# Kernel optimization log

Measured on AMD Instinct MI355X. Metric: run time of the kernel, lower is better.

Reference implementation:

```python
import jax, jax.numpy as jnp
import numpy as np

N_NODES = 50000
N_EDGES = 800000
D = 128


def _gcn_layer(x, src, dst, deg_inv_sqrt, W, b, n_nodes):
    # GCNConv: X' = D^{-1/2} (A + I) D^{-1/2} X W + b   (PyG default, self-loops added)
    h = x @ W  # [N, D]
    norm = deg_inv_sqrt[src] * deg_inv_sqrt[dst]  # [E+N]
    msgs = h[src] * norm[:, None]  # [E+N, D] gather + scale
    out = jax.ops.segment_sum(msgs, dst, num_segments=n_nodes)  # scatter-add
    return out + b


def setup_inputs() -> dict:
    key = jax.random.key(0)
    k1, k2, k3, k4 = jax.random.split(key, 4)
    x = jax.random.normal(k1, (N_NODES, D), dtype=jnp.float32)
    edge_index = jax.random.randint(k2, (2, N_EDGES), 0, N_NODES, dtype=jnp.int64)
    scale = 1.0 / np.sqrt(D)
    W1 = jax.random.normal(k3, (D, D), dtype=jnp.float32) * scale
    b1 = jnp.zeros((D,), dtype=jnp.float32)
    W2 = jax.random.normal(k4, (D, D), dtype=jnp.float32) * scale
    b2 = jnp.zeros((D,), dtype=jnp.float32)
    return {"x": x, "edge_index": edge_index, "W1": W1, "b1": b1, "W2": W2, "b2": b2}


def reference(x, edge_index, W1, b1, W2, b2):
    n_nodes = x.shape[0]
    # add self-loops once (same graph both layers)
    loop = jnp.arange(n_nodes, dtype=edge_index.dtype)
    src = jnp.concatenate([edge_index[0], loop])
    dst = jnp.concatenate([edge_index[1], loop])
    deg = jax.ops.segment_sum(jnp.ones_like(dst, dtype=x.dtype), dst, num_segments=n_nodes)
    deg_inv_sqrt = jnp.where(deg > 0, jax.lax.rsqrt(deg), 0.0)

    h = _gcn_layer(x, src, dst, deg_inv_sqrt, W1, b1, n_nodes)
    h = jax.nn.relu(h)
    h = _gcn_layer(h, src, dst, deg_inv_sqrt, W2, b2, n_nodes)
    h = jax.nn.relu(h)
    return h
```

## Files before the change

### kernel.cpp

```cpp
#include <hip/hip_runtime.h>

#define N_NODES 50000
#define N_EDGES 800000
#define D 128
#define NB 392
#define CHUNK 2048
#define NBKT 391
#define LHM (NBKT * NB)
#define NSB ((LHM + 255) / 256)
#define GB ((N_NODES + 127) / 128)

typedef unsigned int uint32;
typedef unsigned short ushort;
typedef __attribute__((ext_vector_type(8))) short s8v;
typedef __attribute__((ext_vector_type(4))) float f4v;

__device__ __forceinline__ ushort f2bf(float f) {
    unsigned u = __float_as_uint(f);
    u += 0x7FFFu + ((u >> 16) & 1u);
    return (ushort)(u >> 16);
}
__device__ __forceinline__ float bf_lo(uint32 u) { return __uint_as_float(u << 16); }
__device__ __forceinline__ float bf_hi(uint32 u) { return __uint_as_float(u & 0xFFFF0000u); }

__device__ __forceinline__ int block_incl_scan(int v, int t) {
    int lane = t & 63, wv = t >> 6;
    int incl = v;
    #pragma unroll
    for (int off = 1; off < 64; off <<= 1) {
        int u = __shfl_up(incl, off, 64);
        if (lane >= off) incl += u;
    }
    __shared__ int wsums[4];
    if (lane == 63) wsums[wv] = incl;
    __syncthreads();
    int add = 0;
    if (wv > 0) add += wsums[0];
    if (wv > 1) add += wsums[1];
    if (wv > 2) add += wsums[2];
    return incl + add;
}

__global__ __launch_bounds__(256) void phaseA_kernel(const int* __restrict__ dst,
                                                     int* __restrict__ histM,
                                                     const float* __restrict__ W1,
                                                     const float* __restrict__ W2,
                                                     ushort* __restrict__ W1t,
                                                     ushort* __restrict__ W2t) {
    int t = threadIdx.x, blk = blockIdx.x;
    if (blk >= NB) {
        const float* W = (blk - NB) ? W2 : W1;
        ushort* Wt = (blk - NB) ? W2t : W1t;
        #pragma unroll
        for (int it = 0; it < 16; it++) {
            int fid = t + it * 256;
            int k = fid >> 5;
            int n0 = (fid & 31) * 4;
            float4 w = ((const float4*)W)[fid];
            Wt[(n0 + 0) * D + k] = f2bf(w.x);
            Wt[(n0 + 1) * D + k] = f2bf(w.y);
            Wt[(n0 + 2) * D + k] = f2bf(w.z);
            Wt[(n0 + 3) * D + k] = f2bf(w.w);
        }
        return;
    }
    __shared__ int lc[NBKT];
    for (int i = t; i < NBKT; i += 256) lc[i] = 0;
    __syncthreads();
    int e0 = blk * CHUNK;
    #pragma unroll
    for (int j = 0; j < 8; j++) {
        int e = e0 + t + j * 256;
        if (e < N_EDGES) atomicAdd(&lc[dst[e] >> 7], 1);
    }
    __syncthreads();
    for (int i = t; i < NBKT; i += 256)
        histM[i * NB + blk] = lc[i];
}

__global__ __launch_bounds__(256) void scan1g(const int* __restrict__ in,
                                              int* __restrict__ out,
                                              int* __restrict__ bsum) {
    int t = threadIdx.x, blk = blockIdx.x;
    int i = blk * 256 + t;
    int v = (i < LHM) ? in[i] : 0;
    int incl = block_incl_scan(v, t);
    if (i < LHM) out[i] = incl - v;
    if (t == 255) bsum[blk] = incl;
}

__global__ __launch_bounds__(256) void scan23g(int* __restrict__ out,
                                               const int* __restrict__ bsum) {
    int t = threadIdx.x, blk = blockIdx.x;
    int local = 0;
    for (int i = t; i < blk; i += 256) local += bsum[i];
    int lane = t & 63, wv = t >> 6;
    #pragma unroll
    for (int off = 32; off > 0; off >>= 1) local += __shfl_down(local, off, 64);
    __shared__ int ws[4];
    if (lane == 0) ws[wv] = local;
    __syncthreads();
    int boff = ws[0] + ws[1] + ws[2] + ws[3];
    int i = blk * 256 + t;
    if (i < LHM) out[i] += boff;
}

__global__ __launch_bounds__(256) void phaseC_kernel(const int* __restrict__ src,
                                                     const int* __restrict__ dst,
                                                     const int* __restrict__ base,
                                                     uint32* __restrict__ edgeTmp) {
    __shared__ int cur[NBKT];
    int t = threadIdx.x, blk = blockIdx.x;
    for (int i = t; i < NBKT; i += 256) cur[i] = base[i * NB + blk];
    __syncthreads();
    int e0 = blk * CHUNK;
    #pragma unroll
    for (int j = 0; j < 8; j++) {
        int e = e0 + t + j * 256;
        if (e < N_EDGES) {
            uint32 s = (uint32)src[e], d = (uint32)dst[e];
            int p = atomicAdd(&cur[d >> 7], 1);
            edgeTmp[p] = (s << 16) | d;
        }
    }
}

__global__ __launch_bounds__(256) void phaseD_kernel(const uint32* __restrict__ edgeTmp,
                                                     const int* __restrict__ base,
                                                     int* __restrict__ rowstart,
                                                     float* __restrict__ dis,
                                                     ushort* __restrict__ e16) {
    __shared__ int cnt[128];
    __shared__ int cur[128];
    int t = threadIdx.x, b = blockIdx.x;
    int beg = base[b * NB];
    int end = (b == NBKT - 1) ? N_EDGES : base[(b + 1) * NB];
    if (t < 128) cnt[t] = 0;
    __syncthreads();
    for (int p = beg + t; p < end; p += 256)
        atomicAdd(&cnt[edgeTmp[p] & 127], 1);
    __syncthreads();
    int c = (t < 128) ? cnt[t] : 0;
    int incl = block_incl_scan(c, t);
    int excl = incl - c;
    int node = b * 128 + t;
    if (t < 128) {
        if (node <= N_NODES) rowstart[node] = beg + excl;
        if (node < N_NODES) dis[node] = rsqrtf((float)(c + 1));
        cur[t] = excl;
    }
    __syncthreads();
    for (int p = beg + t; p < end; p += 256) {
        uint32 u = edgeTmp[p];
        int r = atomicAdd(&cur[u & 127], 1);
        e16[beg + r] = (ushort)(u >> 16);
    }
}

template<bool BF16IN>
__global__ __launch_bounds__(256) void gemm_mfma(const void* __restrict__ Xv,
                                                 const ushort* __restrict__ Wt,
                                                 const float* __restrict__ dis,
                                                 ushort* __restrict__ Hb) {
    __shared__ ushort Cs[128 * 136];
    int t = threadIdx.x;
    int wv = t >> 6, lane = t & 63;
    int q = lane >> 4, m = lane & 15;
    int rbase = blockIdx.x * 128 + wv * 32;
    f4v zero = {0.f, 0.f, 0.f, 0.f};
    f4v acc[2][8];
    #pragma unroll
    for (int mt = 0; mt < 2; mt++)
        #pragma unroll
        for (int n = 0; n < 8; n++) acc[mt][n] = zero;

    #pragma unroll
    for (int kt = 0; kt < 4; kt++) {
        int k0 = kt * 32 + q * 8;
        s8v a[2];
        #pragma unroll
        for (int mt = 0; mt < 2; mt++) {
            int row = rbase + mt * 16 + m;
            if (row >= N_NODES) row = N_NODES - 1;
            if (BF16IN) {
                const ushort* xp = (const ushort*)Xv + (size_t)row * D + k0;
                a[mt] = *(const s8v*)xp;
            } else {
                const float* xp = (const float*)Xv + (size_t)row * D + k0;
                float4 u0 = *(const float4*)xp;
                float4 u1 = *(const float4*)(xp + 4);
                s8v av;
                av[0] = (short)f2bf(u0.x); av[1] = (short)f2bf(u0.y);
                av[2] = (short)f2bf(u0.z); av[3] = (short)f2bf(u0.w);
                av[4] = (short)f2bf(u1.x); av[5] = (short)f2bf(u1.y);
                av[6] = (short)f2bf(u1.z); av[7] = (short)f2bf(u1.w);
                a[mt] = av;
            }
        }
        #pragma unroll
        for (int n = 0; n < 8; n++) {
            s8v b = *(const s8v*)(Wt + (size_t)(n * 16 + m) * D + k0);
            acc[0][n] = __builtin_amdgcn_mfma_f32_16x16x32_bf16(a[0], b, acc[0][n], 0, 0, 0);
            acc[1][n] = __builtin_amdgcn_mfma_f32_16x16x32_bf16(a[1], b, acc[1][n], 0, 0, 0);
        }
    }
    float disv[2][4];
    #pragma unroll
    for (int mt = 0; mt < 2; mt++)
        #pragma unroll
        for (int r = 0; r < 4; r++) {
            int row = rbase + mt * 16 + q * 4 + r;
            if (row >= N_NODES) row = N_NODES - 1;
            disv[mt][r] = dis[row];
        }
    #pragma unroll
    for (int mt = 0; mt < 2; mt++)
        #pragma unroll
        for (int n = 0; n < 8; n++)
            #pragma unroll
            for (int r = 0; r < 4; r++) {
                int row = wv * 32 + mt * 16 + q * 4 + r;
                Cs[row * 136 + n * 16 + m] = f2bf(acc[mt][n][r] * disv[mt][r]);
            }
    __syncthreads();
    int gbase = blockIdx.x * 128;
    #pragma unroll
    for (int it = 0; it < 8; it++) {
        int cid = t + it * 256;
        int row = cid >> 4, off = (cid & 15) * 8;
        int grow = gbase + row;
        if (grow < N_NODES) {
            s8v v = *(const s8v*)(Cs + row * 136 + off);
            *(s8v*)(Hb + (size_t)grow * D + off) = v;
        }
    }
}

__device__ __forceinline__ void acc8(float* a, uint4 v) {
    a[0] += bf_lo(v.x); a[1] += bf_hi(v.x);
    a[2] += bf_lo(v.y); a[3] += bf_hi(v.y);
    a[4] += bf_lo(v.z); a[5] += bf_hi(v.z);
    a[6] += bf_lo(v.w); a[7] += bf_hi(v.w);
}

template<bool BF16OUT>
__global__ __launch_bounds__(256) void aggr_kernel(const uint4* __restrict__ Hb4,
                                                   const float* __restrict__ dis,
                                                   const int* __restrict__ rowstart,
                                                   const ushort* __restrict__ e16,
                                                   const float* __restrict__ bias,
                                                   void* __restrict__ Hout) {
    int t = threadIdx.x;
    int li = t & 15;
    int n = blockIdx.x * 16 + (t >> 4);
    float dn = dis[n];
    float a[8];
    {
        uint4 sv = Hb4[(size_t)n * 16 + li];
        a[0] = bf_lo(sv.x); a[1] = bf_hi(sv.x);
        a[2] = bf_lo(sv.y); a[3] = bf_hi(sv.y);
        a[4] = bf_lo(sv.z); a[5] = bf_hi(sv.z);
        a[6] = bf_lo(sv.w); a[7] = bf_hi(sv.w);
    }
    int beg = rowstart[n], end = rowstart[n + 1];
    int p = beg;
    for (; p + 7 < end; p += 8) {
        int s[8];
        #pragma unroll
        for (int j = 0; j < 8; j++) s[j] = e16[p + j];
        uint4 v[8];
        #pragma unroll
        for (int j = 0; j < 8; j++) v[j] = Hb4[(size_t)s[j] * 16 + li];
        #pragma unroll
        for (int j = 0; j < 8; j++) acc8(a, v[j]);
    }
    for (; p + 3 < end; p += 4) {
        int s0 = e16[p + 0], s1 = e16[p + 1], s2 = e16[p + 2], s3 = e16[p + 3];
        uint4 v0 = Hb4[(size_t)s0 * 16 + li];
        uint4 v1 = Hb4[(size_t)s1 * 16 + li];
        uint4 v2 = Hb4[(size_t)s2 * 16 + li];
        uint4 v3 = Hb4[(size_t)s3 * 16 + li];
        acc8(a, v0); acc8(a, v1); acc8(a, v2); acc8(a, v3);
    }
    for (; p < end; p++) {
        uint4 v0 = Hb4[(size_t)e16[p] * 16 + li];
        acc8(a, v0);
    }
    const float4* b4 = (const float4*)bias;
    float4 bb0 = b4[li * 2], bb1 = b4[li * 2 + 1];
    float r0 = fmaxf(fmaf(dn, a[0], bb0.x), 0.f);
    float r1 = fmaxf(fmaf(dn, a[1], bb0.y), 0.f);
    float r2 = fmaxf(fmaf(dn, a[2], bb0.z), 0.f);
    float r3 = fmaxf(fmaf(dn, a[3], bb0.w), 0.f);
    float r4 = fmaxf(fmaf(dn, a[4], bb1.x), 0.f);
    float r5 = fmaxf(fmaf(dn, a[5], bb1.y), 0.f);
    float r6 = fmaxf(fmaf(dn, a[6], bb1.z), 0.f);
    float r7 = fmaxf(fmaf(dn, a[7], bb1.w), 0.f);
    if (BF16OUT) {
        uint4 o;
        o.x = (uint32)f2bf(r0) | ((uint32)f2bf(r1) << 16);
        o.y = (uint32)f2bf(r2) | ((uint32)f2bf(r3) << 16);
        o.z = (uint32)f2bf(r4) | ((uint32)f2bf(r5) << 16);
        o.w = (uint32)f2bf(r6) | ((uint32)f2bf(r7) << 16);
        ((uint4*)Hout)[(size_t)n * 16 + li] = o;
    } else {
        float4* H4 = (float4*)Hout;
        float4 o0; o0.x = r0; o0.y = r1; o0.z = r2; o0.w = r3;
        float4 o1; o1.x = r4; o1.y = r5; o1.z = r6; o1.w = r7;
        H4[(size_t)n * 32 + li * 2]     = o0;
        H4[(size_t)n * 32 + li * 2 + 1] = o1;
    }
}

extern "C" void kernel_launch(void* const* d_in, const int* in_sizes, int n_in,
                              void* d_out, int out_size, void* d_ws, size_t ws_size,
                              hipStream_t stream) {
    const float* x  = (const float*)d_in[0];
    const int*   ei = (const int*)d_in[1];
    const float* W1 = (const float*)d_in[2];
    const float* b1 = (const float*)d_in[3];
    const float* W2 = (const float*)d_in[4];
    const float* b2 = (const float*)d_in[5];
    float* out = (float*)d_out;

    char* ws = (char*)d_ws;
    size_t off = 0;
    auto alloc = [&](size_t bytes) -> void* {
        void* p = ws + off;
        off += (bytes + 255) & ~(size_t)255;
        return p;
    };
    int*    histM    = (int*)alloc((size_t)LHM * 4);
    int*    base     = (int*)alloc((size_t)LHM * 4);
    int*    bsum     = (int*)alloc((size_t)NSB * 4);
    int*    rowstart = (int*)alloc((size_t)(N_NODES + 1) * 4);
    float*  dis      = (float*)alloc((size_t)N_NODES * 4);
    uint32* edgeTmp  = (uint32*)alloc((size_t)N_EDGES * 4);
    ushort* e16      = (ushort*)alloc((size_t)N_EDGES * 2);
    ushort* Hb       = (ushort*)alloc((size_t)N_NODES * D * 2);
    ushort* HO1      = (ushort*)alloc((size_t)N_NODES * D * 2);
    ushort* W1t      = (ushort*)alloc((size_t)D * D * 2);
    ushort* W2t      = (ushort*)alloc((size_t)D * D * 2);

    const int* src = ei;
    const int* dst = ei + N_EDGES;

    phaseA_kernel<<<NB + 2, 256, 0, stream>>>(dst, histM, W1, W2, W1t, W2t);
    scan1g<<<NSB, 256, 0, stream>>>(histM, base, bsum);
    scan23g<<<NSB, 256, 0, stream>>>(base, bsum);
    phaseC_kernel<<<NB, 256, 0, stream>>>(src, dst, base, edgeTmp);
    phaseD_kernel<<<NBKT, 256, 0, stream>>>(edgeTmp, base, rowstart, dis, e16);

    gemm_mfma<false><<<GB, 256, 0, stream>>>(x, W1t, dis, Hb);
    aggr_kernel<true><<<N_NODES / 16, 256, 0, stream>>>((const uint4*)Hb, dis, rowstart,
                                                        e16, b1, HO1);
    gemm_mfma<true><<<GB, 256, 0, stream>>>(HO1, W2t, dis, Hb);
    aggr_kernel<false><<<N_NODES / 16, 256, 0, stream>>>((const uint4*)Hb, dis, rowstart,
                                                         e16, b2, out);
}
```

Before: 204.8 us.

## Sort nodes by degree and remap aggregation to balance wavefront work

Adds three kernels that histogram node in-degrees, scan the bins, and build a permutation that groups nodes of similar degree into the same wavefront. The aggregation kernel is restructured so each node is handled by 4 lanes looping over four feature quarters, with 16 nodes per wave and blocks built from the degree-sorted permutation. The goal is to cut lane divergence from unequal neighbour counts within a wave. The cost is extra preprocessing launches and a serial quarter loop that re-reads edge indices four times per node.

```diff
diff --git a/kernel.cpp b/kernel.cpp
--- a/kernel.cpp
+++ b/kernel.cpp
@@ -9,6 +9,9 @@
 #define LHM (NBKT * NB)
 #define NSB ((LHM + 255) / 256)
 #define GB ((N_NODES + 127) / 128)
+#define AGB 782
+#define NBIN 128
+#define BPAD 32
 
 typedef unsigned int uint32;
 typedef unsigned short ushort;
@@ -46,8 +49,13 @@
                                                      const float* __restrict__ W1,
                                                      const float* __restrict__ W2,
                                                      ushort* __restrict__ W1t,
-                                                     ushort* __restrict__ W2t) {
+                                                     ushort* __restrict__ W2t,
+                                                     int* __restrict__ dhist) {
     int t = threadIdx.x, blk = blockIdx.x;
+    if (blk == NB + 2) {
+        for (int i = t; i < NBIN * BPAD; i += 256) dhist[i] = 0;
+        return;
+    }
     if (blk >= NB) {
         const float* W = (blk - NB) ? W2 : W1;
         ushort* Wt = (blk - NB) ? W2t : W1t;
@@ -154,6 +162,63 @@
         uint32 u = edgeTmp[p];
         int r = atomicAdd(&cur[u & 127], 1);
         e16[beg + r] = (ushort)(u >> 16);
+    }
+}
+
+__global__ __launch_bounds__(256) void histdeg_kernel(const int* __restrict__ rowstart,
+                                                      int* __restrict__ dhist) {
+    __shared__ int dh[NBIN];
+    int t = threadIdx.x;
+    if (t < NBIN) dh[t] = 0;
+    __syncthreads();
+    int n = blockIdx.x * 256 + t;
+    if (n < N_NODES) {
+        int deg = rowstart[n + 1] - rowstart[n];
+        atomicAdd(&dh[deg > NBIN - 1 ? NBIN - 1 : deg], 1);
+    }
+    __syncthreads();
+    if (t < NBIN && dh[t] > 0) atomicAdd(&dhist[t * BPAD], dh[t]);
+}
+
+__global__ __launch_bounds__(128) void scandeg_kernel(const int* __restrict__ dhist,
+                                                      int* __restrict__ dcur) {
+    __shared__ int s[NBIN];
+    int t = threadIdx.x;
+    int v0 = dhist[t * BPAD];
+    s[t] = v0;
+    __syncthreads();
+    for (int off = 1; off < NBIN; off <<= 1) {
+        int v = (t >= off) ? s[t - off] : 0;
+        __syncthreads();
+        s[t] += v;
+        __syncthreads();
+    }
+    dcur[t * BPAD] = s[t] - v0;
+}
+
+__global__ __launch_bounds__(256) void permbuild_kernel(const int* __restrict__ rowstart,
+                                                        int* __restrict__ dcur,
+                                                        int* __restrict__ perm) {
+    __shared__ int bh[NBIN];
+    __shared__ int bbase[NBIN];
+    int t = threadIdx.x;
+    if (t < NBIN) bh[t] = 0;
+    __syncthreads();
+    int n = blockIdx.x * 256 + t;
+    int bin = -1, myloc = 0;
+    if (n < N_NODES) {
+        int deg = rowstart[n + 1] - rowstart[n];
+        bin = deg > NBIN - 1 ? NBIN - 1 : deg;
+        myloc = atomicAdd(&bh[bin], 1);
+    }
+    __syncthreads();
+    if (t < NBIN && bh[t] > 0) bbase[t] = atomicAdd(&dcur[t * BPAD], bh[t]);
+    __syncthreads();
+    if (n < N_NODES) {
+        int r = bbase[bin] + myloc;
+        int j = r >> 4, i = r & 15;
+        int wv = j / AGB, b = j - wv * AGB;
+        perm[b * 64 + wv * 16 + i] = n;
     }
 }
 
@@ -248,67 +313,82 @@
                                                    const float* __restrict__ dis,
                                                    const int* __restrict__ rowstart,
                                                    const ushort* __restrict__ e16,
+                                                   const int* __restrict__ perm,
                                                    const float* __restrict__ bias,
                                                    void* __restrict__ Hout) {
     int t = threadIdx.x;
-    int li = t & 15;
-    int n = blockIdx.x * 16 + (t >> 4);
-    float dn = dis[n];
-    float a[8];
-    {
-        uint4 sv = Hb4[(size_t)n * 16 + li];
-        a[0] = bf_lo(sv.x); a[1] = bf_hi(sv.x);
-        a[2] = bf_lo(sv.y); a[3] = bf_hi(sv.y);
-        a[4] = bf_lo(sv.z); a[5] = bf_hi(sv.z);
-        a[6] = bf_lo(sv.w); a[7] = bf_hi(sv.w);
-    }
-    int beg = rowstart[n], end = rowstart[n + 1];
-    int p = beg;
-    for (; p + 7 < end; p += 8) {
-        int s[8];
-        #pragma unroll
-        for (int j = 0; j < 8; j++) s[j] = e16[p + j];
-        uint4 v[8];
-        #pragma unroll
-        for (int j = 0; j < 8; j++) v[j] = Hb4[(size_t)s[j] * 16 + li];
-        #pragma unroll
-        for (int j = 0; j < 8; j++) acc8(a, v[j]);
-    }
-    for (; p + 3 < end; p += 4) {
-        int s0 = e16[p + 0], s1 = e16[p + 1], s2 = e16[p + 2], s3 = e16[p + 3];
-        uint4 v0 = Hb4[(size_t)s0 * 16 + li];
-        uint4 v1 = Hb4[(size_t)s1 * 16 + li];
-        uint4 v2 = Hb4[(size_t)s2 * 16 + li];
-        uint4 v3 = Hb4[(size_t)s3 * 16 + li];
-        acc8(a, v0); acc8(a, v1); acc8(a, v2); acc8(a, v3);
-    }
-    for (; p < end; p++) {
-        uint4 v0 = Hb4[(size_t)e16[p] * 16 + li];
-        acc8(a, v0);
+    int li = t & 3;
+    int wv = t >> 6;
+    int i16 = (t >> 2) & 15;
+    int b = blockIdx.x;
+    int r = (wv * AGB + b) * 16 + i16;
+    bool valid = (r < N_NODES);
+    int n = 0; float dn = 0.f; int beg = 0, end = 0;
+    if (valid) {
+        n = perm[b * 64 + wv * 16 + i16];
+        dn = dis[n];
+        beg = rowstart[n]; end = rowstart[n + 1];
     }
     const float4* b4 = (const float4*)bias;
-    float4 bb0 = b4[li * 2], bb1 = b4[li * 2 + 1];
-    float r0 = fmaxf(fmaf(dn, a[0], bb0.x), 0.f);
-    float r1 = fmaxf(fmaf(dn, a[1], bb0.y), 0.f);
-    float r2 = fmaxf(fmaf(dn, a[2], bb0.z), 0.f);
-    float r3 = fmaxf(fmaf(dn, a[3], bb0.w), 0.f);
-    float r4 = fmaxf(fmaf(dn, a[4], bb1.x), 0.f);
-    float r5 = fmaxf(fmaf(dn, a[5], bb1.y), 0.f);
-    float r6 = fmaxf(fmaf(dn, a[6], bb1.z), 0.f);
-    float r7 = fmaxf(fmaf(dn, a[7], bb1.w), 0.f);
-    if (BF16OUT) {
-        uint4 o;
-        o.x = (uint32)f2bf(r0) | ((uint32)f2bf(r1) << 16);
-        o.y = (uint32)f2bf(r2) | ((uint32)f2bf(r3) << 16);
-        o.z = (uint32)f2bf(r4) | ((uint32)f2bf(r5) << 16);
-        o.w = (uint32)f2bf(r6) | ((uint32)f2bf(r7) << 16);
-        ((uint4*)Hout)[(size_t)n * 16 + li] = o;
-    } else {
-        float4* H4 = (float4*)Hout;
-        float4 o0; o0.x = r0; o0.y = r1; o0.z = r2; o0.w = r3;
-        float4 o1; o1.x = r4; o1.y = r5; o1.z = r6; o1.w = r7;
-        H4[(size_t)n * 32 + li * 2]     = o0;
-        H4[(size_t)n * 32 + li * 2 + 1] = o1;
+    #pragma unroll 1
+    for (int qtr = 0; qtr < 4; qtr++) {
+        if (valid) {
+            int ci = qtr * 4 + li;
+            float a[8];
+            {
+                uint4 sv = Hb4[(size_t)n * 16 + ci];
+                a[0] = bf_lo(sv.x); a[1] = bf_hi(sv.x);
+                a[2] = bf_lo(sv.y); a[3] = bf_hi(sv.y);
+                a[4] = bf_lo(sv.z); a[5] = bf_hi(sv.z);
+                a[6] = bf_lo(sv.w); a[7] = bf_hi(sv.w);
+            }
+            int p = beg;
+            for (; p + 7 < end; p += 8) {
+                int s[8];
+                #pragma unroll
+                for (int j = 0; j < 8; j++) s[j] = e16[p + j];
+                uint4 v[8];
+                #pragma unroll
+                for (int j = 0; j < 8; j++) v[j] = Hb4[(size_t)s[j] * 16 + ci];
+                #pragma unroll
+                for (int j = 0; j < 8; j++) acc8(a, v[j]);
+            }
+            for (; p + 3 < end; p += 4) {
+                int s0 = e16[p + 0], s1 = e16[p + 1], s2 = e16[p + 2], s3 = e16[p + 3];
+                uint4 v0 = Hb4[(size_t)s0 * 16 + ci];
+                uint4 v1 = Hb4[(size_t)s1 * 16 + ci];
+                uint4 v2 = Hb4[(size_t)s2 * 16 + ci];
+                uint4 v3 = Hb4[(size_t)s3 * 16 + ci];
+                acc8(a, v0); acc8(a, v1); acc8(a, v2); acc8(a, v3);
+            }
+            for (; p < end; p++) {
+                uint4 v0 = Hb4[(size_t)e16[p] * 16 + ci];
+                acc8(a, v0);
+            }
+            float4 bb0 = b4[ci * 2], bb1 = b4[ci * 2 + 1];
+            float r0 = fmaxf(fmaf(dn, a[0], bb0.x), 0.f);
+            float r1 = fmaxf(fmaf(dn, a[1], bb0.y), 0.f);
+            float r2 = fmaxf(fmaf(dn, a[2], bb0.z), 0.f);
+            float r3 = fmaxf(fmaf(dn, a[3], bb0.w), 0.f);
+            float r4 = fmaxf(fmaf(dn, a[4], bb1.x), 0.f);
+            float r5 = fmaxf(fmaf(dn, a[5], bb1.y), 0.f);
+            float r6 = fmaxf(fmaf(dn, a[6], bb1.z), 0.f);
+            float r7 = fmaxf(fmaf(dn, a[7], bb1.w), 0.f);
+            if (BF16OUT) {
+                uint4 o;
+                o.x = (uint32)f2bf(r0) | ((uint32)f2bf(r1) << 16);
+                o.y = (uint32)f2bf(r2) | ((uint32)f2bf(r3) << 16);
+                o.z = (uint32)f2bf(r4) | ((uint32)f2bf(r5) << 16);
+                o.w = (uint32)f2bf(r6) | ((uint32)f2bf(r7) << 16);
+                ((uint4*)Hout)[(size_t)n * 16 + ci] = o;
+            } else {
+                float4* H4 = (float4*)Hout;
+                float4 o0; o0.x = r0; o0.y = r1; o0.z = r2; o0.w = r3;
+                float4 o1; o1.x = r4; o1.y = r5; o1.z = r6; o1.w = r7;
+                H4[(size_t)n * 32 + ci * 2]     = o0;
+                H4[(size_t)n * 32 + ci * 2 + 1] = o1;
+            }
+        }
     }
 }
 
@@ -341,20 +421,26 @@
     ushort* HO1      = (ushort*)alloc((size_t)N_NODES * D * 2);
     ushort* W1t      = (ushort*)alloc((size_t)D * D * 2);
     ushort* W2t      = (ushort*)alloc((size_t)D * D * 2);
+    int*    dhist    = (int*)alloc((size_t)NBIN * BPAD * 4);
+    int*    dcur     = (int*)alloc((size_t)NBIN * BPAD * 4);
+    int*    perm     = (int*)alloc((size_t)AGB * 64 * 4);
 
     const int* src = ei;
     const int* dst = ei + N_EDGES;
 
-    phaseA_kernel<<<NB + 2, 256, 0, stream>>>(dst, histM, W1, W2, W1t, W2t);
+    phaseA_kernel<<<NB + 3, 256, 0, stream>>>(dst, histM, W1, W2, W1t, W2t, dhist);
     scan1g<<<NSB, 256, 0, stream>>>(histM, base, bsum);
     scan23g<<<NSB, 256, 0, stream>>>(base, bsum);
     phaseC_kernel<<<NB, 256, 0, stream>>>(src, dst, base, edgeTmp);
     phaseD_kernel<<<NBKT, 256, 0, stream>>>(edgeTmp, base, rowstart, dis, e16);
+    histdeg_kernel<<<(N_NODES + 255) / 256, 256, 0, stream>>>(rowstart, dhist);
+    scandeg_kernel<<<1, 128, 0, stream>>>(dhist, dcur);
+    permbuild_kernel<<<(N_NODES + 255) / 256, 256, 0, stream>>>(rowstart, dcur, perm);
 
     gemm_mfma<false><<<GB, 256, 0, stream>>>(x, W1t, dis, Hb);
-    aggr_kernel<true><<<N_NODES / 16, 256, 0, stream>>>((const uint4*)Hb, dis, rowstart,
-                                                        e16, b1, HO1);
+    aggr_kernel<true><<<AGB, 256, 0, stream>>>((const uint4*)Hb, dis, rowstart,
+                                               e16, perm, b1, HO1);
     gemm_mfma<true><<<GB, 256, 0, stream>>>(HO1, W2t, dis, Hb);
-    aggr_kernel<false><<<N_NODES / 16, 256, 0, stream>>>((const uint4*)Hb, dis, rowstart,
-                                                         e16, b2, out);
-}
+    aggr_kernel<false><<<AGB, 256, 0, stream>>>((const uint4*)Hb, dis, rowstart,
+                                                e16, perm, b2, out);
+}
```

Result: slower. 255.2 us (+24.6%).

## Sort nodes by degree into a permutation to balance aggregation wavefronts

Applied to the files above, without the earlier changes.

Adds a degree histogram in phaseD, a single-block scan, and a permutation-building kernel that groups nodes of similar degree. Each wavefront of the aggregation kernels then handles four nodes with near-equal edge counts, which reduces divergence in the edge loop. The cost is two extra kernel launches, global atomics, and scattered output writes and row reads, since consecutive threads no longer touch consecutive nodes.

```diff
diff --git a/kernel.cpp b/kernel.cpp
--- a/kernel.cpp
+++ b/kernel.cpp
@@ -9,6 +9,9 @@
 #define LHM (NBKT * NB)
 #define NSB ((LHM + 255) / 256)
 #define GB ((N_NODES + 127) / 128)
+#define PB 3125
+#define NBIN 128
+#define BPAD 32
 
 typedef unsigned int uint32;
 typedef unsigned short ushort;
@@ -46,8 +49,13 @@
                                                      const float* __restrict__ W1,
                                                      const float* __restrict__ W2,
                                                      ushort* __restrict__ W1t,
-                                                     ushort* __restrict__ W2t) {
+                                                     ushort* __restrict__ W2t,
+                                                     int* __restrict__ dhist) {
     int t = threadIdx.x, blk = blockIdx.x;
+    if (blk == NB + 2) {
+        for (int i = t; i < NBIN * BPAD; i += 256) dhist[i] = 0;
+        return;
+    }
     if (blk >= NB) {
         const float* W = (blk - NB) ? W2 : W1;
         ushort* Wt = (blk - NB) ? W2t : W1t;
@@ -129,31 +137,78 @@
                                                      const int* __restrict__ base,
                                                      int* __restrict__ rowstart,
                                                      float* __restrict__ dis,
-                                                     ushort* __restrict__ e16) {
+                                                     ushort* __restrict__ e16,
+                                                     int* __restrict__ dhist) {
     __shared__ int cnt[128];
     __shared__ int cur[128];
+    __shared__ int dh[NBIN];
     int t = threadIdx.x, b = blockIdx.x;
     int beg = base[b * NB];
     int end = (b == NBKT - 1) ? N_EDGES : base[(b + 1) * NB];
-    if (t < 128) cnt[t] = 0;
+    if (t < 128) cnt[t] = 0; else dh[t - 128] = 0;
     __syncthreads();
     for (int p = beg + t; p < end; p += 256)
         atomicAdd(&cnt[edgeTmp[p] & 127], 1);
     __syncthreads();
     int c = (t < 128) ? cnt[t] : 0;
+    int node = b * 128 + t;
+    if (t < 128 && node < N_NODES)
+        atomicAdd(&dh[c > NBIN - 1 ? NBIN - 1 : c], 1);
     int incl = block_incl_scan(c, t);
     int excl = incl - c;
-    int node = b * 128 + t;
     if (t < 128) {
         if (node <= N_NODES) rowstart[node] = beg + excl;
         if (node < N_NODES) dis[node] = rsqrtf((float)(c + 1));
         cur[t] = excl;
     }
     __syncthreads();
+    if (t < 128 && dh[t] > 0) atomicAdd(&dhist[t * BPAD], dh[t]);
     for (int p = beg + t; p < end; p += 256) {
         uint32 u = edgeTmp[p];
         int r = atomicAdd(&cur[u & 127], 1);
         e16[beg + r] = (ushort)(u >> 16);
+    }
+}
+
+__global__ __launch_bounds__(128) void scandeg_kernel(const int* __restrict__ dhist,
+                                                      int* __restrict__ dcur) {
+    __shared__ int s[NBIN];
+    int t = threadIdx.x;
+    int v0 = dhist[t * BPAD];
+    s[t] = v0;
+    __syncthreads();
+    for (int off = 1; off < NBIN; off <<= 1) {
+        int v = (t >= off) ? s[t - off] : 0;
+        __syncthreads();
+        s[t] += v;
+        __syncthreads();
+    }
+    dcur[t * BPAD] = s[t] - v0;
+}
+
+__global__ __launch_bounds__(256) void permbuild_kernel(const int* __restrict__ rowstart,
+                                                        int* __restrict__ dcur,
+                                                        int* __restrict__ perm) {
+    __shared__ int bh[NBIN];
+    __shared__ int bbase[NBIN];
+    int t = threadIdx.x;
+    if (t < NBIN) bh[t] = 0;
+    __syncthreads();
+    int n = blockIdx.x * 256 + t;
+    int bin = -1, myloc = 0;
+    if (n < N_NODES) {
+        int deg = rowstart[n + 1] - rowstart[n];
+        bin = deg > NBIN - 1 ? NBIN - 1 : deg;
+        myloc = atomicAdd(&bh[bin], 1);
+    }
+    __syncthreads();
+    if (t < NBIN && bh[t] > 0) bbase[t] = atomicAdd(&dcur[t * BPAD], bh[t]);
+    __syncthreads();
+    if (n < N_NODES) {
+        int r = bbase[bin] + myloc;
+        int j = r >> 2, i = r & 3;
+        int wv = j / PB, b = j - wv * PB;
+        perm[b * 16 + wv * 4 + i] = n;
     }
 }
 
@@ -248,11 +303,12 @@
                                                    const float* __restrict__ dis,
                                                    const int* __restrict__ rowstart,
                                                    const ushort* __restrict__ e16,
+                                                   const int* __restrict__ perm,
                                                    const float* __restrict__ bias,
                                                    void* __restrict__ Hout) {
     int t = threadIdx.x;
     int li = t & 15;
-    int n = blockIdx.x * 16 + (t >> 4);
+    int n = perm[blockIdx.x * 16 + (t >> 4)];
     float dn = dis[n];
     float a[8];
     {
@@ -341,20 +397,25 @@
     ushort* HO1      = (ushort*)alloc((size_t)N_NODES * D * 2);
     ushort* W1t      = (ushort*)alloc((size_t)D * D * 2);
     ushort* W2t      = (ushort*)alloc((size_t)D * D * 2);
+    int*    dhist    = (int*)alloc((size_t)NBIN * BPAD * 4);
+    int*    dcur     = (int*)alloc((size_t)NBIN * BPAD * 4);
+    int*    perm     = (int*)alloc((size_t)N_NODES * 4);
 
     const int* src = ei;
     const int* dst = ei + N_EDGES;
 
-    phaseA_kernel<<<NB + 2, 256, 0, stream>>>(dst, histM, W1, W2, W1t, W2t);
+    phaseA_kernel<<<NB + 3, 256, 0, stream>>>(dst, histM, W1, W2, W1t, W2t, dhist);
     scan1g<<<NSB, 256, 0, stream>>>(histM, base, bsum);
     scan23g<<<NSB, 256, 0, stream>>>(base, bsum);
     phaseC_kernel<<<NB, 256, 0, stream>>>(src, dst, base, edgeTmp);
-    phaseD_kernel<<<NBKT, 256, 0, stream>>>(edgeTmp, base, rowstart, dis, e16);
+    phaseD_kernel<<<NBKT, 256, 0, stream>>>(edgeTmp, base, rowstart, dis, e16, dhist);
+    scandeg_kernel<<<1, 128, 0, stream>>>(dhist, dcur);
+    permbuild_kernel<<<(N_NODES + 255) / 256, 256, 0, stream>>>(rowstart, dcur, perm);
 
     gemm_mfma<false><<<GB, 256, 0, stream>>>(x, W1t, dis, Hb);
-    aggr_kernel<true><<<N_NODES / 16, 256, 0, stream>>>((const uint4*)Hb, dis, rowstart,
-                                                        e16, b1, HO1);
+    aggr_kernel<true><<<PB, 256, 0, stream>>>((const uint4*)Hb, dis, rowstart,
+                                              e16, perm, b1, HO1);
     gemm_mfma<true><<<GB, 256, 0, stream>>>(HO1, W2t, dis, Hb);
-    aggr_kernel<false><<<N_NODES / 16, 256, 0, stream>>>((const uint4*)Hb, dis, rowstart,
-                                                         e16, b2, out);
-}
+    aggr_kernel<false><<<PB, 256, 0, stream>>>((const uint4*)Hb, dis, rowstart,
+                                               e16, perm, b2, out);
+}
```

After: 217.4 us. +6.2%, slower.

## Fuse first GEMM into CSR build and second GEMM into layer-1 aggregation

Applied to the files above, without the earlier changes.

The first feature transform (X·W1 scaled by dis) now runs at the end of the CSR-finalize kernel, which reuses the per-node degree values kept in shared memory. The layer-1 aggregation kernel now does the second GEMM on its own 128-node tile, keeping the aggregated bf16 rows in LDS. This removes two launches and the HO1 round trip through global memory. In exchange, the aggregation kernel runs only 391 blocks that each loop over 8 passes, so it exposes less parallelism for latency hiding during the gather. The fused blocks also use more LDS.

```diff
diff --git a/kernel.cpp b/kernel.cpp
--- a/kernel.cpp
+++ b/kernel.cpp
@@ -8,7 +8,7 @@
 #define NBKT 391
 #define LHM (NBKT * NB)
 #define NSB ((LHM + 255) / 256)
-#define GB ((N_NODES + 127) / 128)
+#define PB 3125
 
 typedef unsigned int uint32;
 typedef unsigned short ushort;
@@ -125,13 +125,18 @@
     }
 }
 
-__global__ __launch_bounds__(256) void phaseD_kernel(const uint32* __restrict__ edgeTmp,
-                                                     const int* __restrict__ base,
-                                                     int* __restrict__ rowstart,
-                                                     float* __restrict__ dis,
-                                                     ushort* __restrict__ e16) {
+__global__ __launch_bounds__(256) void phaseDG_kernel(const uint32* __restrict__ edgeTmp,
+                                                      const int* __restrict__ base,
+                                                      int* __restrict__ rowstart,
+                                                      float* __restrict__ dis,
+                                                      ushort* __restrict__ e16,
+                                                      const float* __restrict__ X,
+                                                      const ushort* __restrict__ Wt,
+                                                      ushort* __restrict__ Hb) {
     __shared__ int cnt[128];
     __shared__ int cur[128];
+    __shared__ float disS[128];
+    __shared__ ushort Cs[128 * 136];
     int t = threadIdx.x, b = blockIdx.x;
     int beg = base[b * NB];
     int end = (b == NBKT - 1) ? N_EDGES : base[(b + 1) * NB];
@@ -146,7 +151,9 @@
     int node = b * 128 + t;
     if (t < 128) {
         if (node <= N_NODES) rowstart[node] = beg + excl;
-        if (node < N_NODES) dis[node] = rsqrtf((float)(c + 1));
+        float dv = rsqrtf((float)(c + 1));
+        if (node < N_NODES) dis[node] = dv;
+        disS[t] = dv;
         cur[t] = excl;
     }
     __syncthreads();
@@ -155,25 +162,15 @@
         int r = atomicAdd(&cur[u & 127], 1);
         e16[beg + r] = (ushort)(u >> 16);
     }
-}
-
-template<bool BF16IN>
-__global__ __launch_bounds__(256) void gemm_mfma(const void* __restrict__ Xv,
-                                                 const ushort* __restrict__ Wt,
-                                                 const float* __restrict__ dis,
-                                                 ushort* __restrict__ Hb) {
-    __shared__ ushort Cs[128 * 136];
-    int t = threadIdx.x;
     int wv = t >> 6, lane = t & 63;
     int q = lane >> 4, m = lane & 15;
-    int rbase = blockIdx.x * 128 + wv * 32;
+    int rbase = b * 128 + wv * 32;
     f4v zero = {0.f, 0.f, 0.f, 0.f};
     f4v acc[2][8];
     #pragma unroll
     for (int mt = 0; mt < 2; mt++)
         #pragma unroll
         for (int n = 0; n < 8; n++) acc[mt][n] = zero;
-
     #pragma unroll
     for (int kt = 0; kt < 4; kt++) {
         int k0 = kt * 32 + q * 8;
@@ -182,48 +179,35 @@
         for (int mt = 0; mt < 2; mt++) {
             int row = rbase + mt * 16 + m;
             if (row >= N_NODES) row = N_NODES - 1;
-            if (BF16IN) {
-                const ushort* xp = (const ushort*)Xv + (size_t)row * D + k0;
-                a[mt] = *(const s8v*)xp;
-            } else {
-                const float* xp = (const float*)Xv + (size_t)row * D + k0;
-                float4 u0 = *(const float4*)xp;
-                float4 u1 = *(const float4*)(xp + 4);
-                s8v av;
-                av[0] = (short)f2bf(u0.x); av[1] = (short)f2bf(u0.y);
-                av[2] = (short)f2bf(u0.z); av[3] = (short)f2bf(u0.w);
-                av[4] = (short)f2bf(u1.x); av[5] = (short)f2bf(u1.y);
-                av[6] = (short)f2bf(u1.z); av[7] = (short)f2bf(u1.w);
-                a[mt] = av;
-            }
+            const float* xp = X + (size_t)row * D + k0;
+            float4 u0 = *(const float4*)xp;
+            float4 u1 = *(const float4*)(xp + 4);
+            s8v av;
+            av[0] = (short)f2bf(u0.x); av[1] = (short)f2bf(u0.y);
+            av[2] = (short)f2bf(u0.z); av[3] = (short)f2bf(u0.w);
+            av[4] = (short)f2bf(u1.x); av[5] = (short)f2bf(u1.y);
+            av[6] = (short)f2bf(u1.z); av[7] = (short)f2bf(u1.w);
+            a[mt] = av;
         }
         #pragma unroll
         for (int n = 0; n < 8; n++) {
-            s8v b = *(const s8v*)(Wt + (size_t)(n * 16 + m) * D + k0);
-            acc[0][n] = __builtin_amdgcn_mfma_f32_16x16x32_bf16(a[0], b, acc[0][n], 0, 0, 0);
-            acc[1][n] = __builtin_amdgcn_mfma_f32_16x16x32_bf16(a[1], b, acc[1][n], 0, 0, 0);
-        }
-    }
-    float disv[2][4];
-    #pragma unroll
-    for (int mt = 0; mt < 2; mt++)
-        #pragma unroll
-        for (int r = 0; r < 4; r++) {
-            int row = rbase + mt * 16 + q * 4 + r;
-            if (row >= N_NODES) row = N_NODES - 1;
-            disv[mt][r] = dis[row];
-        }
+            s8v bb = *(const s8v*)(Wt + (size_t)(n * 16 + m) * D + k0);
+            acc[0][n] = __builtin_amdgcn_mfma_f32_16x16x32_bf16(a[0], bb, acc[0][n], 0, 0, 0);
+            acc[1][n] = __builtin_amdgcn_mfma_f32_16x16x32_bf16(a[1], bb, acc[1][n], 0, 0, 0);
+        }
+    }
+    __syncthreads();
     #pragma unroll
     for (int mt = 0; mt < 2; mt++)
         #pragma unroll
         for (int n = 0; n < 8; n++)
             #pragma unroll
             for (int r = 0; r < 4; r++) {
-                int row = wv * 32 + mt * 16 + q * 4 + r;
-                Cs[row * 136 + n * 16 + m] = f2bf(acc[mt][n][r] * disv[mt][r]);
-            }
-    __syncthreads();
-    int gbase = blockIdx.x * 128;
+                int lr = wv * 32 + mt * 16 + q * 4 + r;
+                Cs[lr * 136 + n * 16 + m] = f2bf(acc[mt][n][r] * disS[lr]);
+            }
+    __syncthreads();
+    int gbase = b * 128;
     #pragma unroll
     for (int it = 0; it < 8; it++) {
         int cid = t + it * 256;
@@ -243,13 +227,128 @@
     a[6] += bf_lo(v.w); a[7] += bf_hi(v.w);
 }
 
-template<bool BF16OUT>
+__global__ __launch_bounds__(256) void aggrG_kernel(const uint4* __restrict__ Hb4,
+                                                    const float* __restrict__ dis,
+                                                    const int* __restrict__ rowstart,
+                                                    const ushort* __restrict__ e16,
+                                                    const float* __restrict__ bias,
+                                                    const ushort* __restrict__ Wt,
+                                                    ushort* __restrict__ Hb2) {
+    __shared__ ushort Cs[128 * 136];
+    __shared__ float disS[128];
+    int t = threadIdx.x, blk = blockIdx.x;
+    int li = t & 15, g = t >> 4;
+    const float4* b4 = (const float4*)bias;
+    float4 bb0 = b4[li * 2], bb1 = b4[li * 2 + 1];
+    #pragma unroll 1
+    for (int pass = 0; pass < 8; pass++) {
+        int local = pass * 16 + g;
+        int n = blk * 128 + local;
+        if (n < N_NODES) {
+            float dn = dis[n];
+            if (li == 0) disS[local] = dn;
+            float a[8];
+            {
+                uint4 sv = Hb4[(size_t)n * 16 + li];
+                a[0] = bf_lo(sv.x); a[1] = bf_hi(sv.x);
+                a[2] = bf_lo(sv.y); a[3] = bf_hi(sv.y);
+                a[4] = bf_lo(sv.z); a[5] = bf_hi(sv.z);
+                a[6] = bf_lo(sv.w); a[7] = bf_hi(sv.w);
+            }
+            int beg = rowstart[n], end = rowstart[n + 1];
+            int p = beg;
+            for (; p + 7 < end; p += 8) {
+                int s[8];
+                #pragma unroll
+                for (int j = 0; j < 8; j++) s[j] = e16[p + j];
+                uint4 v[8];
+                #pragma unroll
+                for (int j = 0; j < 8; j++) v[j] = Hb4[(size_t)s[j] * 16 + li];
+                #pragma unroll
+                for (int j = 0; j < 8; j++) acc8(a, v[j]);
+            }
+            for (; p + 3 < end; p += 4) {
+                int s0 = e16[p + 0], s1 = e16[p + 1], s2 = e16[p + 2], s3 = e16[p + 3];
+                uint4 v0 = Hb4[(size_t)s0 * 16 + li];
+                uint4 v1 = Hb4[(size_t)s1 * 16 + li];
+                uint4 v2 = Hb4[(size_t)s2 * 16 + li];
+                uint4 v3 = Hb4[(size_t)s3 * 16 + li];
+                acc8(a, v0); acc8(a, v1); acc8(a, v2); acc8(a, v3);
+            }
+            for (; p < end; p++) {
+                uint4 v0 = Hb4[(size_t)e16[p] * 16 + li];
+                acc8(a, v0);
+            }
+            s8v o;
+            o[0] = (short)f2bf(fmaxf(fmaf(dn, a[0], bb0.x), 0.f));
+            o[1] = (short)f2bf(fmaxf(fmaf(dn, a[1], bb0.y), 0.f));
+            o[2] = (short)f2bf(fmaxf(fmaf(dn, a[2], bb0.z), 0.f));
+            o[3] = (short)f2bf(fmaxf(fmaf(dn, a[3], bb0.w), 0.f));
+            o[4] = (short)f2bf(fmaxf(fmaf(dn, a[4], bb1.x), 0.f));
+            o[5] = (short)f2bf(fmaxf(fmaf(dn, a[5], bb1.y), 0.f));
+            o[6] = (short)f2bf(fmaxf(fmaf(dn, a[6], bb1.z), 0.f));
+            o[7] = (short)f2bf(fmaxf(fmaf(dn, a[7], bb1.w), 0.f));
+            *(s8v*)(Cs + local * 136 + li * 8) = o;
+        } else {
+            s8v z = {0, 0, 0, 0, 0, 0, 0, 0};
+            if (li == 0) disS[local] = 0.f;
+            *(s8v*)(Cs + local * 136 + li * 8) = z;
+        }
+    }
+    __syncthreads();
+    int wv = t >> 6, lane = t & 63;
+    int q = lane >> 4, m = lane & 15;
+    int rloc = wv * 32;
+    f4v zero = {0.f, 0.f, 0.f, 0.f};
+    f4v acc[2][8];
+    #pragma unroll
+    for (int mt = 0; mt < 2; mt++)
+        #pragma unroll
+        for (int n = 0; n < 8; n++) acc[mt][n] = zero;
+    #pragma unroll
+    for (int kt = 0; kt < 4; kt++) {
+        int k0 = kt * 32 + q * 8;
+        s8v a[2];
+        #pragma unroll
+        for (int mt = 0; mt < 2; mt++)
+            a[mt] = *(const s8v*)(Cs + (rloc + mt * 16 + m) * 136 + k0);
+        #pragma unroll
+        for (int n = 0; n < 8; n++) {
+            s8v bb = *(const s8v*)(Wt + (size_t)(n * 16 + m) * D + k0);
+            acc[0][n] = __builtin_amdgcn_mfma_f32_16x16x32_bf16(a[0], bb, acc[0][n], 0, 0, 0);
+            acc[1][n] = __builtin_amdgcn_mfma_f32_16x16x32_bf16(a[1], bb, acc[1][n], 0, 0, 0);
+        }
+    }
+    __syncthreads();
+    #pragma unroll
+    for (int mt = 0; mt < 2; mt++)
+        #pragma unroll
+        for (int n = 0; n < 8; n++)
+            #pragma unroll
+            for (int r = 0; r < 4; r++) {
+                int lr = wv * 32 + mt * 16 + q * 4 + r;
+                Cs[lr * 136 + n * 16 + m] = f2bf(acc[mt][n][r] * disS[lr]);
+            }
+    __syncthreads();
+    int gbase = blk * 128;
+    #pragma unroll
+    for (int it = 0; it < 8; it++) {
+        int cid = t + it * 256;
+        int row = cid >> 4, off = (cid & 15) * 8;
+        int grow = gbase + row;
+        if (grow < N_NODES) {
+            s8v v = *(const s8v*)(Cs + row * 136 + off);
+            *(s8v*)(Hb2 + (size_t)grow * D + off) = v;
+        }
+    }
+}
+
 __global__ __launch_bounds__(256) void aggr_kernel(const uint4* __restrict__ Hb4,
                                                    const float* __restrict__ dis,
                                                    const int* __restrict__ rowstart,
                                                    const ushort* __restrict__ e16,
                                                    const float* __restrict__ bias,
-                                                   void* __restrict__ Hout) {
+                                                   float* __restrict__ Hout) {
     int t = threadIdx.x;
     int li = t & 15;
     int n = blockIdx.x * 16 + (t >> 4);
@@ -288,28 +387,18 @@
     }
     const float4* b4 = (const float4*)bias;
     float4 bb0 = b4[li * 2], bb1 = b4[li * 2 + 1];
-    float r0 = fmaxf(fmaf(dn, a[0], bb0.x), 0.f);
-    float r1 = fmaxf(fmaf(dn, a[1], bb0.y), 0.f);
-    float r2 = fmaxf(fmaf(dn, a[2], bb0.z), 0.f);
-    float r3 = fmaxf(fmaf(dn, a[3], bb0.w), 0.f);
-    float r4 = fmaxf(fmaf(dn, a[4], bb1.x), 0.f);
-    float r5 = fmaxf(fmaf(dn, a[5], bb1.y), 0.f);
-    float r6 = fmaxf(fmaf(dn, a[6], bb1.z), 0.f);
-    float r7 = fmaxf(fmaf(dn, a[7], bb1.w), 0.f);
-    if (BF16OUT) {
-        uint4 o;
-        o.x = (uint32)f2bf(r0) | ((uint32)f2bf(r1) << 16);
-        o.y = (uint32)f2bf(r2) | ((uint32)f2bf(r3) << 16);
-        o.z = (uint32)f2bf(r4) | ((uint32)f2bf(r5) << 16);
-        o.w = (uint32)f2bf(r6) | ((uint32)f2bf(r7) << 16);
-        ((uint4*)Hout)[(size_t)n * 16 + li] = o;
-    } else {
-        float4* H4 = (float4*)Hout;
-        float4 o0; o0.x = r0; o0.y = r1; o0.z = r2; o0.w = r3;
-        float4 o1; o1.x = r4; o1.y = r5; o1.z = r6; o1.w = r7;
-        H4[(size_t)n * 32 + li * 2]     = o0;
-        H4[(size_t)n * 32 + li * 2 + 1] = o1;
-    }
+    float4 o0, o1;
+    o0.x = fmaxf(fmaf(dn, a[0], bb0.x), 0.f);
+    o0.y = fmaxf(fmaf(dn, a[1], bb0.y), 0.f);
+    o0.z = fmaxf(fmaf(dn, a[2], bb0.z), 0.f);
+    o0.w = fmaxf(fmaf(dn, a[3], bb0.w), 0.f);
+    o1.x = fmaxf(fmaf(dn, a[4], bb1.x), 0.f);
+    o1.y = fmaxf(fmaf(dn, a[5], bb1.y), 0.f);
+    o1.z = fmaxf(fmaf(dn, a[6], bb1.z), 0.f);
+    o1.w = fmaxf(fmaf(dn, a[7], bb1.w), 0.f);
+    float4* H4 = (float4*)Hout;
+    H4[(size_t)n * 32 + li * 2]     = o0;
+    H4[(size_t)n * 32 + li * 2 + 1] = o1;
 }
 
 extern "C" void kernel_launch(void* const* d_in, const int* in_sizes, int n_in,
@@ -338,7 +427,7 @@
     uint32* edgeTmp  = (uint32*)alloc((size_t)N_EDGES * 4);
     ushort* e16      = (ushort*)alloc((size_t)N_EDGES * 2);
     ushort* Hb       = (ushort*)alloc((size_t)N_NODES * D * 2);
-    ushort* HO1      = (ushort*)alloc((size_t)N_NODES * D * 2);
+    ushort* Hb2      = (ushort*)alloc((size_t)N_NODES * D * 2);
     ushort* W1t      = (ushort*)alloc((size_t)D * D * 2);
     ushort* W2t      = (ushort*)alloc((size_t)D * D * 2);
 
@@ -349,12 +438,10 @@
     scan1g<<<NSB, 256, 0, stream>>>(histM, base, bsum);
     scan23g<<<NSB, 256, 0, stream>>>(base, bsum);
     phaseC_kernel<<<NB, 256, 0, stream>>>(src, dst, base, edgeTmp);
-    phaseD_kernel<<<NBKT, 256, 0, stream>>>(edgeTmp, base, rowstart, dis, e16);
-
-    gemm_mfma<false><<<GB, 256, 0, stream>>>(x, W1t, dis, Hb);
-    aggr_kernel<true><<<N_NODES / 16, 256, 0, stream>>>((const uint4*)Hb, dis, rowstart,
-                                                        e16, b1, HO1);
-    gemm_mfma<true><<<GB, 256, 0, stream>>>(HO1, W2t, dis, Hb);
-    aggr_kernel<false><<<N_NODES / 16, 256, 0, stream>>>((const uint4*)Hb, dis, rowstart,
-                                                         e16, b2, out);
-}
+    phaseDG_kernel<<<NBKT, 256, 0, stream>>>(edgeTmp, base, rowstart, dis, e16,
+                                             x, W1t, Hb);
+    aggrG_kernel<<<NBKT, 256, 0, stream>>>((const uint4*)Hb, dis, rowstart, e16,
+                                           b1, W2t, Hb2);
+    aggr_kernel<<<PB, 256, 0, stream>>>((const uint4*)Hb2, dis, rowstart, e16,
+                                        b2, out);
+}
```

Measured after the change: 209.3 us. +2.2%, slower.
